# Kernel tuning notes

Hardware: AMD Instinct MI355X
Metric: run time of the kernel (lower is better)

## Reference

```python
import jax, jax.numpy as jnp
import numpy as np


def setup_inputs() -> dict:
    key = jax.random.key(0)
    k1, k2, k3 = jax.random.split(key, 3)
    B, T, E = 4, 2048, 1024
    x = jax.random.normal(k1, (B, T, E), dtype=jnp.float32)
    # torch nn.Linear weight layout: [out_features, in_features]
    w_qkv = jax.random.normal(k2, (3 * E, E), dtype=jnp.float32) * (E ** -0.5)
    w_out = jax.random.normal(k3, (E, E), dtype=jnp.float32) * (E ** -0.5)
    return {"x": x, "w_qkv": w_qkv, "w_out": w_out}


def reference(x, w_qkv, w_out):
    B, T, E = x.shape
    H = 16
    D = E // H  # head_dim
    # QKV projection (Linear, bias=False): x @ W.T -> [B,T,3E]
    qkv = jnp.einsum('bte,fe->btf', x, w_qkv)
    qkv = qkv.reshape(B, T, 3, H, D).transpose(2, 0, 3, 1, 4)  # [3,B,H,T,D]
    q, k, v = qkv[0], qkv[1], qkv[2]
    scale = 1.0 / jnp.sqrt(jnp.asarray(D, dtype=x.dtype))
    att = jnp.einsum('bhqd,bhkd->bhqk', q, k) * scale  # [B,H,T,T]
    causal = jnp.tril(jnp.ones((T, T), dtype=bool))
    att = jnp.where(causal[None, None], att, jnp.asarray(-jnp.inf, dtype=att.dtype))
    att = jax.nn.softmax(att, axis=-1)
    # dropout = 0.0 (eval-mode): identity
    y = jnp.einsum('bhqk,bhkd->bhqd', att, v)  # [B,H,T,D]
    y = y.transpose(0, 2, 1, 3).reshape(B, T, E)
    return jnp.einsum('bte,fe->btf', y, w_out)
```

## Files before the change

### kernel.cpp

```cpp
#include <hip/hip_runtime.h>

typedef __bf16 bf16x8 __attribute__((ext_vector_type(8)));
typedef __bf16 bf16x4 __attribute__((ext_vector_type(4)));
typedef __bf16 bf16x2 __attribute__((ext_vector_type(2)));
typedef float f32x4 __attribute__((ext_vector_type(4)));
typedef float f32x16 __attribute__((ext_vector_type(16)));
typedef unsigned short ushortx8 __attribute__((ext_vector_type(8)));
typedef unsigned short ushortx4 __attribute__((ext_vector_type(4)));
typedef unsigned int uint32x4v __attribute__((ext_vector_type(4)));

#define DEVI static __device__ __forceinline__

DEVI unsigned short f2bf(float f) {
  unsigned int u = __builtin_bit_cast(unsigned int, f);
  u += 0x7FFFu + ((u >> 16) & 1u);
  return (unsigned short)(u >> 16);
}

DEVI bf16x8 ld8(const unsigned short* p) {
  return __builtin_bit_cast(bf16x8, *(const ushortx8*)p);
}

DEVI void gll16(const unsigned short* g, unsigned short* l) {
  __builtin_amdgcn_global_load_lds((const __attribute__((address_space(1))) void*)g,
                                   (__attribute__((address_space(3))) void*)l, 16, 0, 0);
}

#define MFMA16(a, b, c) __builtin_amdgcn_mfma_f32_16x16x32_bf16(a, b, c, 0, 0, 0)
#define MFMA32(a, b, c) __builtin_amdgcn_mfma_f32_32x32x16_bf16(a, b, c, 0, 0, 0)

DEVI unsigned pkbf(float lo, float hi) {
  bf16x2 v;
  v[0] = (__bf16)lo;
  v[1] = (__bf16)hi;
  return __builtin_bit_cast(unsigned, v);
}

DEVI float swaphalf_max(float x) {
  unsigned xu = __builtin_bit_cast(unsigned, x);
  auto pr = __builtin_amdgcn_permlane32_swap(xu, xu, false, false);
  return fmaxf(__builtin_bit_cast(float, (unsigned)pr[0]),
               __builtin_bit_cast(float, (unsigned)pr[1]));
}

DEVI float swaphalf_add(float x) {
  unsigned xu = __builtin_bit_cast(unsigned, x);
  auto pr = __builtin_amdgcn_permlane32_swap(xu, xu, false, false);
  return __builtin_bit_cast(float, (unsigned)pr[0]) +
         __builtin_bit_cast(float, (unsigned)pr[1]);
}

#define SB 4
#define ST 2048
#define SE 1024
#define SH 16
#define SD 64
#define QSCALE 0.18033688011112042f
#define DMTHR 11.541560327111708f

__global__ void cvt_f32_bf16(const float* __restrict__ in, unsigned short* __restrict__ out, int n4) {
  int i = blockIdx.x * blockDim.x + threadIdx.x;
  if (i >= n4) return;
  float4 v = ((const float4*)in)[i];
  ushortx4 o;
  o.x = f2bf(v.x); o.y = f2bf(v.y); o.z = f2bf(v.z); o.w = f2bf(v.w);
  ((ushortx4*)out)[i] = o;
}

template<int EPI>
__global__ __launch_bounds__(256, 2) void gemm_nt(
    const unsigned short* __restrict__ A, const unsigned short* __restrict__ Bw,
    float* __restrict__ Cf,
    unsigned short* __restrict__ Qo, unsigned short* __restrict__ Ko,
    unsigned short* __restrict__ VTo,
    int M, int N, int K) {
  __shared__ unsigned short As[128 * 64];
  __shared__ unsigned short Bs[128 * 64];
  const int tid = threadIdx.x;
  const int lane = tid & 63;
  const int w = tid >> 6;
  const int wr = w >> 1, wc = w & 1;
  const int r16 = lane & 15, g = lane >> 4;

  const int nwg = gridDim.x * gridDim.y;
  const int lin = blockIdx.x + blockIdx.y * gridDim.x;
  const int wg = (lin & 7) * (nwg >> 3) + (lin >> 3);
  const int bx = wg % gridDim.x, by = wg / gridDim.x;
  const int m0 = by * 128, n0 = bx * 128;

  f32x4 acc[4][4] = {};

  for (int k0 = 0; k0 < K; k0 += 64) {
    __syncthreads();
#pragma unroll
    for (int it = 0; it < 4; ++it) {
      int c = it * 256 + tid;
      int row = c >> 3, cb = (c & 7) * 8;
      gll16(A + (size_t)(m0 + row) * K + k0 + cb, As + c * 8);
    }
#pragma unroll
    for (int it = 0; it < 4; ++it) {
      int c = it * 256 + tid;
      int row = c >> 3, cb = (c & 7) * 8;
      gll16(Bw + (size_t)(n0 + row) * K + k0 + cb, Bs + c * 8);
    }
    __syncthreads();
#pragma unroll
    for (int ks = 0; ks < 2; ++ks) {
      bf16x8 af[4], bfr[4];
#pragma unroll
      for (int mt = 0; mt < 4; ++mt)
        af[mt] = ld8(&As[(wr * 64 + mt * 16 + r16) * 64 + ks * 32 + g * 8]);
#pragma unroll
      for (int nt = 0; nt < 4; ++nt)
        bfr[nt] = ld8(&Bs[(wc * 64 + nt * 16 + r16) * 64 + ks * 32 + g * 8]);
#pragma unroll
      for (int mt = 0; mt < 4; ++mt)
#pragma unroll
        for (int nt = 0; nt < 4; ++nt)
          acc[mt][nt] = MFMA16(af[mt], bfr[nt], acc[mt][nt]);
    }
  }

#pragma unroll
  for (int mt = 0; mt < 4; ++mt) {
#pragma unroll
    for (int nt = 0; nt < 4; ++nt) {
#pragma unroll
      for (int r = 0; r < 4; ++r) {
        int m = m0 + wr * 64 + mt * 16 + g * 4 + r;
        int n = n0 + wc * 64 + nt * 16 + r16;
        float v = acc[mt][nt][r];
        if (EPI == 0) {
          Cf[(size_t)m * N + n] = v;
        } else {
          int b = m >> 11, t = m & (ST - 1);
          int which = n >> 10, h = (n >> 6) & (SH - 1), d = n & (SD - 1);
          int bh = b * SH + h;
          if (which == 0)
            Qo[((size_t)bh * ST + t) * SD + d] = f2bf(v * QSCALE);
          else if (which == 1)
            Ko[((size_t)bh * ST + t) * SD + d] = f2bf(v);
          else
            VTo[((size_t)bh * SD + d) * ST + t] = f2bf(v);
        }
      }
    }
  }
}


DEVI void stage_tile(const unsigned short* gbase, size_t rowstride,
                     unsigned short* lds, int tid) {
#pragma unroll
  for (int it = 0; it < 2; ++it) {
    int c = it * 256 + tid;
    int row = c >> 3, j = c & 7;
    int src = ((j * 16) ^ ((row & 7) << 4)) >> 1;
    gll16(gbase + (size_t)row * rowstride + src, lds + c * 8);
  }
}

DEVI bf16x8 ldswz(const unsigned short* L, int row, int colsh) {
  return ld8(L + row * 64 + ((((colsh * 2) ^ ((row & 7) << 4))) >> 1));
}

__global__ __launch_bounds__(256, 4) void attn_causal(
    const unsigned short* __restrict__ Q, const unsigned short* __restrict__ Kv,
    const unsigned short* __restrict__ VT, unsigned short* __restrict__ Y) {
  __shared__ unsigned short Ks[2][64 * 64];
  __shared__ unsigned short Vs[2][64 * 64];

  const int tid = threadIdx.x;
  const int lane = tid & 63;
  const int w = tid >> 6;
  const int l5 = lane & 31, h = lane >> 5;

  const int lin = blockIdx.x + blockIdx.y * gridDim.x;
  const int xcd = lin & 7;
  const int idx = lin >> 3;
  const int qt = (ST / 128 - 1) - (idx >> 3);
  const int bh = xcd + 8 * (idx & 7);
  const size_t base = (size_t)bh * ST * SD;

  const int q_glob = qt * 128 + w * 32 + l5;
  const int qwmin = qt * 128 + w * 32;

  bf16x8 qf[4];
#pragma unroll
  for (int kk = 0; kk < 4; ++kk)
    qf[kk] = ld8(Q + base + (size_t)q_glob * SD + kk * 16 + h * 8);

  float mrow = -__builtin_inff();
  float lrow = 0.f;
  f32x16 acc[2] = {};

  const int nkv = 2 * qt + 2;
  stage_tile(Kv + base, SD, Ks[0], tid);
  stage_tile(VT + base, ST, Vs[0], tid);
  __syncthreads();

  for (int kvt = 0; kvt < nkv; ++kvt) {
    const int cur = kvt & 1;
    if (kvt + 1 < nkv) {
      stage_tile(Kv + base + (size_t)(kvt + 1) * 64 * SD, SD, Ks[cur ^ 1], tid);
      stage_tile(VT + base + (kvt + 1) * 64, ST, Vs[cur ^ 1], tid);
    }

    const bool active = (kvt * 64) <= (qwmin + 31);
    if (active) {
      f32x16 s0 = {}, s1 = {};
      __builtin_amdgcn_s_setprio(1);
#pragma unroll
      for (int kk = 0; kk < 4; ++kk) {
        bf16x8 k0 = ldswz(Ks[cur], l5, kk * 16 + h * 8);
        s0 = MFMA32(k0, qf[kk], s0);
      }
#pragma unroll
      for (int kk = 0; kk < 4; ++kk) {
        bf16x8 k1 = ldswz(Ks[cur], 32 + l5, kk * 16 + h * 8);
        s1 = MFMA32(k1, qf[kk], s1);
      }
      __builtin_amdgcn_s_setprio(0);

      if (kvt * 64 + 63 > qwmin) {
        const int t0 = kvt * 64 + 4 * h;
#pragma unroll
        for (int reg = 0; reg < 16; ++reg) {
          int t = t0 + (reg & 3) + 8 * (reg >> 2);
          if (t > q_glob) s0[reg] = -__builtin_inff();
          if (t + 32 > q_glob) s1[reg] = -__builtin_inff();
        }
      }

      f32x16 mx;
#pragma unroll
      for (int i = 0; i < 16; ++i) mx[i] = fmaxf(s0[i], s1[i]);
#pragma unroll
      for (int i = 0; i < 8; ++i) mx[i] = fmaxf(mx[i], mx[i + 8]);
#pragma unroll
      for (int i = 0; i < 4; ++i) mx[i] = fmaxf(mx[i], mx[i + 4]);
      float bm = fmaxf(fmaxf(mx[0], mx[1]), fmaxf(mx[2], mx[3]));
      bm = swaphalf_max(bm);

      if (__any(bm > mrow + DMTHR)) {
        float mn = fmaxf(mrow, bm);
        float corr = exp2f(mrow - mn);
        mrow = mn;
        lrow *= corr;
#pragma unroll
        for (int dblk = 0; dblk < 2; ++dblk)
#pragma unroll
          for (int i = 0; i < 16; ++i) acc[dblk][i] *= corr;
      }

#pragma unroll
      for (int i = 0; i < 16; ++i) {
        s0[i] = exp2f(s0[i] - mrow);
        s1[i] = exp2f(s1[i] - mrow);
      }
      f32x16 sm;
#pragma unroll
      for (int i = 0; i < 16; ++i) sm[i] = s0[i] + s1[i];
#pragma unroll
      for (int i = 0; i < 8; ++i) sm[i] += sm[i + 8];
#pragma unroll
      for (int i = 0; i < 4; ++i) sm[i] += sm[i + 4];
      float rs = (sm[0] + sm[1]) + (sm[2] + sm[3]);
      lrow += swaphalf_add(rs);

      bf16x8 pb[2][2];
      auto packblk = [&](const f32x16& S, bf16x8* out) {
        unsigned a = pkbf(S[0], S[1]), b2 = pkbf(S[2], S[3]);
        unsigned c = pkbf(S[4], S[5]), d2 = pkbf(S[6], S[7]);
        auto r0 = __builtin_amdgcn_permlane32_swap(a, c, false, false);
        auto r1 = __builtin_amdgcn_permlane32_swap(b2, d2, false, false);
        uint32x4v w0 = {(unsigned)r0[0], (unsigned)r1[0], (unsigned)r0[1], (unsigned)r1[1]};
        out[0] = __builtin_bit_cast(bf16x8, w0);
        unsigned e = pkbf(S[8], S[9]), f2 = pkbf(S[10], S[11]);
        unsigned g2 = pkbf(S[12], S[13]), h2 = pkbf(S[14], S[15]);
        auto r2 = __builtin_amdgcn_permlane32_swap(e, g2, false, false);
        auto r3 = __builtin_amdgcn_permlane32_swap(f2, h2, false, false);
        uint32x4v w1 = {(unsigned)r2[0], (unsigned)r3[0], (unsigned)r2[1], (unsigned)r3[1]};
        out[1] = __builtin_bit_cast(bf16x8, w1);
      };
      packblk(s0, pb[0]);
      packblk(s1, pb[1]);

      __builtin_amdgcn_s_setprio(1);
#pragma unroll
      for (int dblk = 0; dblk < 2; ++dblk)
#pragma unroll
        for (int tt = 0; tt < 2; ++tt)
#pragma unroll
          for (int sl = 0; sl < 2; ++sl) {
            bf16x8 va = ldswz(Vs[cur], dblk * 32 + l5, tt * 32 + sl * 16 + h * 8);
            acc[dblk] = MFMA32(va, pb[tt][sl], acc[dblk]);
          }
      __builtin_amdgcn_s_setprio(0);
    }

    __syncthreads();
  }

  const int b = bh >> 4, hd = bh & 15;
  const float inv = 1.f / lrow;
#pragma unroll
  for (int dblk = 0; dblk < 2; ++dblk)
#pragma unroll
    for (int rg = 0; rg < 4; ++rg) {
      bf16x4 o;
#pragma unroll
      for (int j = 0; j < 4; ++j) o[j] = (__bf16)(acc[dblk][rg * 4 + j] * inv);
      int d = dblk * 32 + rg * 8 + 4 * h;
      *(ushortx4*)&Y[((size_t)b * ST + q_glob) * SE + hd * SD + d] =
          __builtin_bit_cast(ushortx4, o);
    }
}

extern "C" void kernel_launch(void* const* d_in, const int* in_sizes, int n_in,
                              void* d_out, int out_size, void* d_ws, size_t ws_size,
                              hipStream_t stream) {
  const float* x = (const float*)d_in[0];
  const float* w_qkv = (const float*)d_in[1];
  const float* w_out = (const float*)d_in[2];
  float* out = (float*)d_out;

  const size_t NX = (size_t)SB * ST * SE;
  const size_t NQKV = (size_t)3 * SE * SE;
  const size_t NWO = (size_t)SE * SE;
  const size_t NHD = (size_t)SB * SH * ST * SD;

  unsigned short* xb    = (unsigned short*)d_ws;
  unsigned short* wqkvb = xb + NX;
  unsigned short* woutb = wqkvb + NQKV;
  unsigned short* q     = woutb + NWO;
  unsigned short* k     = q + NHD;
  unsigned short* vT    = k + NHD;
  unsigned short* y     = xb;

  cvt_f32_bf16<<<(int)(NX / 4 + 255) / 256, 256, 0, stream>>>(x, xb, (int)(NX / 4));
  cvt_f32_bf16<<<(int)(NQKV / 4 + 255) / 256, 256, 0, stream>>>(w_qkv, wqkvb, (int)(NQKV / 4));
  cvt_f32_bf16<<<(int)(NWO / 4 + 255) / 256, 256, 0, stream>>>(w_out, woutb, (int)(NWO / 4));

  gemm_nt<1><<<dim3(3 * SE / 128, SB * ST / 128), 256, 0, stream>>>(
      xb, wqkvb, nullptr, q, k, vT, SB * ST, 3 * SE, SE);

  attn_causal<<<dim3(ST / 128, SB * SH), 256, 0, stream>>>(q, k, vT, y);

  gemm_nt<0><<<dim3(SE / 128, SB * ST / 128), 256, 0, stream>>>(
      y, woutb, out, nullptr, nullptr, nullptr, SB * ST, SE, SE);
}
```

Baseline: 203.6 us.

## Double-buffer GEMM LDS tiles and XOR-swizzle them to avoid bank conflicts

The projection GEMM now keeps two LDS buffers for A and B. The next K-tile is prefetched with global_load_lds while the current one is consumed by MFMA, and each iteration needs one barrier instead of two. Tiles are stored with the same XOR swizzle the attention kernel uses, to reduce LDS bank conflicts on the fragment reads. LDS use doubles to 64KB per block, which may limit the target of two blocks per CU.

```diff
diff --git a/kernel.cpp b/kernel.cpp
--- a/kernel.cpp
+++ b/kernel.cpp
@@ -50,6 +50,10 @@
          __builtin_bit_cast(float, (unsigned)pr[1]);
 }
 
+DEVI bf16x8 ldswz(const unsigned short* L, int row, int colsh) {
+  return ld8(L + row * 64 + ((((colsh * 2) ^ ((row & 7) << 4))) >> 1));
+}
+
 #define SB 4
 #define ST 2048
 #define SE 1024
@@ -74,8 +78,8 @@
     unsigned short* __restrict__ Qo, unsigned short* __restrict__ Ko,
     unsigned short* __restrict__ VTo,
     int M, int N, int K) {
-  __shared__ unsigned short As[128 * 64];
-  __shared__ unsigned short Bs[128 * 64];
+  __shared__ unsigned short As[2][128 * 64];
+  __shared__ unsigned short Bs[2][128 * 64];
   const int tid = threadIdx.x;
   const int lane = tid & 63;
   const int w = tid >> 6;
@@ -90,59 +94,71 @@
 
   f32x4 acc[4][4] = {};
 
-  for (int k0 = 0; k0 < K; k0 += 64) {
-    __syncthreads();
+  auto stageAB = [&](int k0, int buf) {
 #pragma unroll
     for (int it = 0; it < 4; ++it) {
       int c = it * 256 + tid;
-      int row = c >> 3, cb = (c & 7) * 8;
-      gll16(A + (size_t)(m0 + row) * K + k0 + cb, As + c * 8);
+      int row = c >> 3, j = c & 7;
+      int src = ((j * 16) ^ ((row & 7) << 4)) >> 1;
+      gll16(A + (size_t)(m0 + row) * K + k0 + src, As[buf] + c * 8);
     }
 #pragma unroll
     for (int it = 0; it < 4; ++it) {
       int c = it * 256 + tid;
-      int row = c >> 3, cb = (c & 7) * 8;
-      gll16(Bw + (size_t)(n0 + row) * K + k0 + cb, Bs + c * 8);
-    }
-    __syncthreads();
+      int row = c >> 3, j = c & 7;
+      int src = ((j * 16) ^ ((row & 7) << 4)) >> 1;
+      gll16(Bw + (size_t)(n0 + row) * K + k0 + src, Bs[buf] + c * 8);
+    }
+  };
+
+  const int nt = K >> 6;
+  stageAB(0, 0);
+  __syncthreads();
+
+  for (int t = 0; t < nt; ++t) {
+    const int cur = t & 1;
+    if (t + 1 < nt) stageAB((t + 1) << 6, cur ^ 1);
+
 #pragma unroll
     for (int ks = 0; ks < 2; ++ks) {
       bf16x8 af[4], bfr[4];
 #pragma unroll
       for (int mt = 0; mt < 4; ++mt)
-        af[mt] = ld8(&As[(wr * 64 + mt * 16 + r16) * 64 + ks * 32 + g * 8]);
-#pragma unroll
-      for (int nt = 0; nt < 4; ++nt)
-        bfr[nt] = ld8(&Bs[(wc * 64 + nt * 16 + r16) * 64 + ks * 32 + g * 8]);
+        af[mt] = ldswz(As[cur], wr * 64 + mt * 16 + r16, ks * 32 + g * 8);
+#pragma unroll
+      for (int nt2 = 0; nt2 < 4; ++nt2)
+        bfr[nt2] = ldswz(Bs[cur], wc * 64 + nt2 * 16 + r16, ks * 32 + g * 8);
 #pragma unroll
       for (int mt = 0; mt < 4; ++mt)
 #pragma unroll
-        for (int nt = 0; nt < 4; ++nt)
-          acc[mt][nt] = MFMA16(af[mt], bfr[nt], acc[mt][nt]);
-    }
+        for (int nt2 = 0; nt2 < 4; ++nt2)
+          acc[mt][nt2] = MFMA16(af[mt], bfr[nt2], acc[mt][nt2]);
+    }
+
+    __syncthreads();
   }
 
 #pragma unroll
   for (int mt = 0; mt < 4; ++mt) {
 #pragma unroll
-    for (int nt = 0; nt < 4; ++nt) {
+    for (int nt2 = 0; nt2 < 4; ++nt2) {
 #pragma unroll
       for (int r = 0; r < 4; ++r) {
         int m = m0 + wr * 64 + mt * 16 + g * 4 + r;
-        int n = n0 + wc * 64 + nt * 16 + r16;
-        float v = acc[mt][nt][r];
+        int n = n0 + wc * 64 + nt2 * 16 + r16;
+        float v = acc[mt][nt2][r];
         if (EPI == 0) {
           Cf[(size_t)m * N + n] = v;
         } else {
-          int b = m >> 11, t = m & (ST - 1);
+          int b = m >> 11, t2 = m & (ST - 1);
           int which = n >> 10, h = (n >> 6) & (SH - 1), d = n & (SD - 1);
           int bh = b * SH + h;
           if (which == 0)
-            Qo[((size_t)bh * ST + t) * SD + d] = f2bf(v * QSCALE);
+            Qo[((size_t)bh * ST + t2) * SD + d] = f2bf(v * QSCALE);
           else if (which == 1)
-            Ko[((size_t)bh * ST + t) * SD + d] = f2bf(v);
+            Ko[((size_t)bh * ST + t2) * SD + d] = f2bf(v);
           else
-            VTo[((size_t)bh * SD + d) * ST + t] = f2bf(v);
+            VTo[((size_t)bh * SD + d) * ST + t2] = f2bf(v);
         }
       }
     }
@@ -159,10 +175,6 @@
     int src = ((j * 16) ^ ((row & 7) << 4)) >> 1;
     gll16(gbase + (size_t)row * rowstride + src, lds + c * 8);
   }
-}
-
-DEVI bf16x8 ldswz(const unsigned short* L, int row, int colsh) {
-  return ld8(L + row * 64 + ((((colsh * 2) ^ ((row & 7) << 4))) >> 1));
 }
 
 __global__ __launch_bounds__(256, 4) void attn_causal(
```

After: 199.2 us. 2.2% less time.

## Load GEMM B fragments directly to registers, swizzle A tile, vectorize V stores

Applied to the files above, without the earlier changes.

The projection GEMM no longer stages the weight tile through LDS. Each wave loads its B fragments straight from global memory into registers and double-buffers them across the two k-halves, prefetching the next iteration. The A tile now uses an XOR-swizzled LDS layout to avoid bank conflicts, and the QKV epilogue hoists index math and writes V-transposed outputs as 4-wide vector stores. This halves LDS use and traffic but adds register pressure and uncoalesced-ish global loads of B that rely on cache reuse across waves.

```diff
diff --git a/kernel.cpp b/kernel.cpp
--- a/kernel.cpp
+++ b/kernel.cpp
@@ -50,6 +50,10 @@
          __builtin_bit_cast(float, (unsigned)pr[1]);
 }
 
+DEVI bf16x8 ldswz(const unsigned short* L, int row, int colsh) {
+  return ld8(L + row * 64 + ((((colsh * 2) ^ ((row & 7) << 4))) >> 1));
+}
+
 #define SB 4
 #define ST 2048
 #define SE 1024
@@ -75,7 +79,6 @@
     unsigned short* __restrict__ VTo,
     int M, int N, int K) {
   __shared__ unsigned short As[128 * 64];
-  __shared__ unsigned short Bs[128 * 64];
   const int tid = threadIdx.x;
   const int lane = tid & 63;
   const int w = tid >> 6;
@@ -88,61 +91,81 @@
   const int bx = wg % gridDim.x, by = wg / gridDim.x;
   const int m0 = by * 128, n0 = bx * 128;
 
+  const unsigned short* Bp = Bw + (size_t)(n0 + wc * 64 + r16) * K + g * 8;
+
   f32x4 acc[4][4] = {};
+  bf16x8 b0[4], b1[4];
+#pragma unroll
+  for (int nt = 0; nt < 4; ++nt) b0[nt] = ld8(Bp + (size_t)nt * 16 * K);
 
   for (int k0 = 0; k0 < K; k0 += 64) {
     __syncthreads();
 #pragma unroll
     for (int it = 0; it < 4; ++it) {
       int c = it * 256 + tid;
-      int row = c >> 3, cb = (c & 7) * 8;
-      gll16(A + (size_t)(m0 + row) * K + k0 + cb, As + c * 8);
-    }
-#pragma unroll
-    for (int it = 0; it < 4; ++it) {
-      int c = it * 256 + tid;
-      int row = c >> 3, cb = (c & 7) * 8;
-      gll16(Bw + (size_t)(n0 + row) * K + k0 + cb, Bs + c * 8);
-    }
+      int row = c >> 3, j = c & 7;
+      int src = ((j * 16) ^ ((row & 7) << 4)) >> 1;
+      gll16(A + (size_t)(m0 + row) * K + k0 + src, As + c * 8);
+    }
+#pragma unroll
+    for (int nt = 0; nt < 4; ++nt) b1[nt] = ld8(Bp + (size_t)nt * 16 * K + k0 + 32);
     __syncthreads();
-#pragma unroll
-    for (int ks = 0; ks < 2; ++ks) {
-      bf16x8 af[4], bfr[4];
-#pragma unroll
-      for (int mt = 0; mt < 4; ++mt)
-        af[mt] = ld8(&As[(wr * 64 + mt * 16 + r16) * 64 + ks * 32 + g * 8]);
+
+    bf16x8 af[4];
+#pragma unroll
+    for (int mt = 0; mt < 4; ++mt) af[mt] = ldswz(As, wr * 64 + mt * 16 + r16, g * 8);
+#pragma unroll
+    for (int mt = 0; mt < 4; ++mt)
+#pragma unroll
+      for (int nt = 0; nt < 4; ++nt) acc[mt][nt] = MFMA16(af[mt], b0[nt], acc[mt][nt]);
+
+    const int kn = (k0 + 64 < K) ? k0 + 64 : 0;
+#pragma unroll
+    for (int nt = 0; nt < 4; ++nt) b0[nt] = ld8(Bp + (size_t)nt * 16 * K + kn);
+
+#pragma unroll
+    for (int mt = 0; mt < 4; ++mt) af[mt] = ldswz(As, wr * 64 + mt * 16 + r16, 32 + g * 8);
+#pragma unroll
+    for (int mt = 0; mt < 4; ++mt)
+#pragma unroll
+      for (int nt = 0; nt < 4; ++nt) acc[mt][nt] = MFMA16(af[mt], b1[nt], acc[mt][nt]);
+  }
+
+  if (EPI == 0) {
+#pragma unroll
+    for (int mt = 0; mt < 4; ++mt)
 #pragma unroll
       for (int nt = 0; nt < 4; ++nt)
-        bfr[nt] = ld8(&Bs[(wc * 64 + nt * 16 + r16) * 64 + ks * 32 + g * 8]);
-#pragma unroll
-      for (int mt = 0; mt < 4; ++mt)
-#pragma unroll
-        for (int nt = 0; nt < 4; ++nt)
-          acc[mt][nt] = MFMA16(af[mt], bfr[nt], acc[mt][nt]);
-    }
-  }
-
-#pragma unroll
-  for (int mt = 0; mt < 4; ++mt) {
-#pragma unroll
-    for (int nt = 0; nt < 4; ++nt) {
-#pragma unroll
-      for (int r = 0; r < 4; ++r) {
-        int m = m0 + wr * 64 + mt * 16 + g * 4 + r;
+#pragma unroll
+        for (int r = 0; r < 4; ++r) {
+          int m = m0 + wr * 64 + mt * 16 + g * 4 + r;
+          int n = n0 + wc * 64 + nt * 16 + r16;
+          Cf[(size_t)m * N + n] = acc[mt][nt][r];
+        }
+  } else {
+    const int which = (n0 + wc * 64) >> 10;
+#pragma unroll
+    for (int mt = 0; mt < 4; ++mt) {
+      const int tb = m0 + wr * 64 + mt * 16 + g * 4;
+      const int b = tb >> 11, t = tb & (ST - 1);
+#pragma unroll
+      for (int nt = 0; nt < 4; ++nt) {
         int n = n0 + wc * 64 + nt * 16 + r16;
-        float v = acc[mt][nt][r];
-        if (EPI == 0) {
-          Cf[(size_t)m * N + n] = v;
+        int h = (n >> 6) & (SH - 1), d = n & (SD - 1);
+        int bh = b * SH + h;
+        if (which == 2) {
+          ushortx4 o;
+#pragma unroll
+          for (int r = 0; r < 4; ++r) o[r] = f2bf(acc[mt][nt][r]);
+          *(ushortx4*)&VTo[((size_t)bh * SD + d) * ST + t] = o;
+        } else if (which == 0) {
+#pragma unroll
+          for (int r = 0; r < 4; ++r)
+            Qo[((size_t)bh * ST + t + r) * SD + d] = f2bf(acc[mt][nt][r] * QSCALE);
         } else {
-          int b = m >> 11, t = m & (ST - 1);
-          int which = n >> 10, h = (n >> 6) & (SH - 1), d = n & (SD - 1);
-          int bh = b * SH + h;
-          if (which == 0)
-            Qo[((size_t)bh * ST + t) * SD + d] = f2bf(v * QSCALE);
-          else if (which == 1)
-            Ko[((size_t)bh * ST + t) * SD + d] = f2bf(v);
-          else
-            VTo[((size_t)bh * SD + d) * ST + t] = f2bf(v);
+#pragma unroll
+          for (int r = 0; r < 4; ++r)
+            Ko[((size_t)bh * ST + t + r) * SD + d] = f2bf(acc[mt][nt][r]);
         }
       }
     }
@@ -159,10 +182,6 @@
     int src = ((j * 16) ^ ((row & 7) << 4)) >> 1;
     gll16(gbase + (size_t)row * rowstride + src, lds + c * 8);
   }
-}
-
-DEVI bf16x8 ldswz(const unsigned short* L, int row, int colsh) {
-  return ld8(L + row * 64 + ((((colsh * 2) ^ ((row & 7) << 4))) >> 1));
 }
 
 __global__ __launch_bounds__(256, 4) void attn_causal(
```

New measurement: 242.2 us. 18.9% more time.
